# Kernel tuning notes

Measured on AMD Instinct MI355X. Metric: run time of the kernel, lower is better.

The kernel has to match this reference:

```python
import jax, jax.numpy as jnp
import numpy as np

N = 100000       # nodes
E = 1000000      # edges
NFEAT = 128
NHID = 256
NCLASS = 40
THRESHOLD = 0.1
EPS = 1e-8


def setup_inputs() -> dict:
    key = jax.random.key(0)
    k = jax.random.split(key, 5)
    x = jax.random.normal(k[0], (N, NFEAT), dtype=jnp.float32)
    row = jax.random.randint(k[1], (E,), 0, N)
    col = jax.random.randint(k[2], (E,), 0, N)
    W1 = jax.random.normal(k[3], (NFEAT, NHID), dtype=jnp.float32) / np.sqrt(NFEAT).astype(np.float32)
    b1 = jnp.zeros((NHID,), jnp.float32)
    W2 = jax.random.normal(k[4], (NHID, NCLASS), dtype=jnp.float32) / np.sqrt(NHID).astype(np.float32)
    b2 = jnp.zeros((NCLASS,), jnp.float32)
    return {"x": x, "row": row, "col": col, "W1": W1, "b1": b1, "W2": W2, "b2": b2}


def _att_coef(feat, row, col, prev_mask=None):
    # per-edge cosine similarity (F.cosine_similarity semantics, eps=1e-8)
    nrm = jnp.maximum(jnp.linalg.norm(feat, axis=1), EPS)  # [N]
    dots = jnp.sum(feat[row] * feat[col], axis=1)          # [E] gather-heavy
    sims = dots / (nrm[row] * nrm[col])
    mask = (sims >= THRESHOLD) & (row != col)
    if prev_mask is not None:
        # edges dropped by a previous att_coef no longer exist in the adj
        mask = mask & prev_mask
    # torch.no_grad in original -> weights are constants
    w = jax.lax.stop_gradient(jnp.where(mask, sims, 0.0))
    return w, mask


def _gcn_conv(x, row, col, w, W, b):
    # PyG GCNConv(add_self_loops=True, normalize=True) with edge weights w.
    # Zero-weight edges are exactly equivalent to removed edges.
    h = x @ W                                             # [N, out]
    deg = jnp.zeros((N,), h.dtype).at[row].add(w) + 1.0   # + self-loop weight 1
    dinv = jax.lax.rsqrt(deg)
    norm = dinv[row] * w * dinv[col]                      # [E]
    out = jnp.zeros((N, h.shape[1]), h.dtype).at[row].add(norm[:, None] * h[col])
    out = out + (dinv * dinv)[:, None] * h                # self-loop contribution
    return out + b


def reference(x, row, col, W1, b1, W2, b2):
    w1, m1 = _att_coef(x, row, col)
    h = _gcn_conv(x, row, col, w1, W1, b1)
    h = jax.nn.relu(h)
    # dropout in eval mode -> identity
    w2, _ = _att_coef(h, row, col, prev_mask=m1)
    out = _gcn_conv(h, row, col, w2, W2, b2)
    return out
```

## Files before the change

kernel.cpp:

```cpp
#include <hip/hip_runtime.h>
#include <hip/hip_bf16.h>
#include <hip/hip_fp16.h>

#define NFEAT 128
#define NHID  256
#define NCLASS 40
#define THRESH 0.1f
#define FEPS   1e-8f
#define GUARD2 4e-3f
#define NSTRIPE 384

struct h2x2 { __half2 a, b; };

typedef _Float16 v2h __attribute__((ext_vector_type(2)));
typedef _Float16 v8h __attribute__((ext_vector_type(8)));
typedef float f32x4 __attribute__((ext_vector_type(4)));

__device__ __forceinline__ float dot2acc(unsigned int a, unsigned int b, float s) {
#if __has_builtin(__builtin_amdgcn_fdot2)
    return __builtin_amdgcn_fdot2(__builtin_bit_cast(v2h, a),
                                  __builtin_bit_cast(v2h, b), s, false);
#else
    float2 fa = __half22float2(__builtin_bit_cast(__half2, a));
    float2 fb = __half22float2(__builtin_bit_cast(__half2, b));
    return s + fa.x * fb.x + fa.y * fb.y;
#endif
}

__device__ __forceinline__ int dot4acc(int a, int b, int acc) {
#if __has_builtin(__builtin_amdgcn_sdot4)
    return __builtin_amdgcn_sdot4(a, b, acc, false);
#else
#pragma unroll
    for (int k = 0; k < 4; ++k) {
        int av = (a << (24 - 8 * k)) >> 24;
        int bv = (b << (24 - 8 * k)) >> 24;
        acc += av * bv;
    }
    return acc;
#endif
}

__device__ __forceinline__ float waveSum(float v) {
#pragma unroll
    for (int off = 32; off > 0; off >>= 1) v += __shfl_xor(v, off, 64);
    return v;
}

__device__ __forceinline__ float qSum16(float v) {
#pragma unroll
    for (int off = 8; off > 0; off >>= 1) v += __shfl_xor(v, off, 64);
    return v;
}

__device__ __forceinline__ float waveMax(float v) {
#pragma unroll
    for (int off = 32; off > 0; off >>= 1) v = fmaxf(v, __shfl_xor(v, off, 64));
    return v;
}

__global__ void k_prep(const float* __restrict__ x,
                       signed char* __restrict__ xq, signed char* __restrict__ xql,
                       float4* __restrict__ meta,
                       float* __restrict__ nrm, float* __restrict__ deg,
                       float* __restrict__ deg2,
                       int* __restrict__ counts, float* __restrict__ nrmsq, int N) {
    int r = (blockIdx.x * blockDim.x + threadIdx.x) >> 6;
    int lane = threadIdx.x & 63;
    if (r >= N) return;
    float2 a = ((const float2*)(x + (size_t)r * NFEAT))[lane];
    float s = waveSum(a.x * a.x + a.y * a.y);
    float nr = fmaxf(sqrtf(s), FEPS);
    float inv = 1.0f / nr;
    float xn0 = a.x * inv, xn1 = a.y * inv;
    float m = waveMax(fmaxf(fabsf(xn0), fabsf(xn1)));
    float t = (m > 0.f) ? 127.f / m : 0.f;
    float sc = m * (1.0f / 127.f);
    int q0 = __float2int_rn(xn0 * t), q1 = __float2int_rn(xn1 * t);
    q0 = max(-127, min(127, q0));
    q1 = max(-127, min(127, q1));
    char2 pk; pk.x = (signed char)q0; pk.y = (signed char)q1;
    ((char2*)(xq + (size_t)r * NFEAT))[lane] = pk;
    float rq = (m > 0.f) ? 256.0f / sc : 0.f;
    int l0 = __float2int_rn((xn0 - sc * (float)q0) * rq);
    int l1 = __float2int_rn((xn1 - sc * (float)q1) * rq);
    l0 = max(-128, min(127, l0));
    l1 = max(-128, min(127, l1));
    char2 pl; pl.x = (signed char)l0; pl.y = (signed char)l1;
    ((char2*)(xql + (size_t)r * NFEAT))[lane] = pl;
    float asum = waveSum((float)(abs(q0) + abs(q1)));
    float axn  = waveSum(fabsf(xn0) + fabsf(xn1));
    if (lane == 0) {
        meta[r] = make_float4(sc, 0.5f * asum + 33.0f, axn, 0.0f);
        nrm[r] = nr;
        deg[r] = 0.0f;
        deg2[r] = 0.0f;
        counts[r] = 0;
        nrmsq[r] = 0.0f;
    }
}

__global__ void k_w1frag(const float* __restrict__ W1f, v8h* __restrict__ w1x) {
    int id = blockIdx.x * 256 + threadIdx.x;
    int frag = id >> 6, lane = id & 63;
    int kb = frag >> 4, ct = frag & 15;
    int kbase = kb * 32 + (lane >> 4) * 8;
    int n = ct * 16 + (lane & 15);
    v8h v;
#pragma unroll
    for (int j = 0; j < 8; ++j)
        v[j] = (_Float16)W1f[(size_t)(kbase + j) * NHID + n];
    w1x[id] = v;
}

__global__ void k_w2frag(const float* __restrict__ W2f, v8h* __restrict__ w2x) {
    int id = blockIdx.x * 256 + threadIdx.x;
    if (id >= 3072) return;
    int part = (id >= 1536) ? 1 : 0;
    int fid = id - part * 1536;
    int frag = fid >> 6, lane = fid & 63;
    int kb = frag / 3, ct = frag % 3;
    int kbase = kb * 32 + (lane >> 4) * 8;
    int n = ct * 16 + (lane & 15);
    v8h v;
#pragma unroll
    for (int j = 0; j < 8; ++j) {
        float wv = (n < NCLASS) ? W2f[(size_t)(kbase + j) * NCLASS + n] : 0.0f;
        _Float16 hi = (_Float16)wv;
        v[j] = part ? (_Float16)(wv - (float)hi) : hi;
    }
    w2x[id] = v;
}

__global__ void k_att1(const float* __restrict__ xf,
                       const signed char* __restrict__ xq,
                       const signed char* __restrict__ xql,
                       const float4* __restrict__ meta,
                       const int* __restrict__ row, const int* __restrict__ col,
                       const float* __restrict__ nrm,
                       float* __restrict__ w1, float* __restrict__ deg,
                       int* __restrict__ counts, int E) {
    int wid = (blockIdx.x * blockDim.x + threadIdx.x) >> 6;
    int lane = threadIdx.x & 63;
    int l8 = lane & 7;
    int e = wid * 8 + (lane >> 3);
    if (e >= E) return;
    int r = row[e], c = col[e];
    int4 qa = ((const int4*)(xq + (size_t)r * NFEAT))[l8];
    int4 qb = ((const int4*)(xq + (size_t)c * NFEAT))[l8];
    int d = 0;
    d = dot4acc(qa.x, qb.x, d);
    d = dot4acc(qa.y, qb.y, d);
    d = dot4acc(qa.z, qb.z, d);
    d = dot4acc(qa.w, qb.w, d);
    d += __shfl_xor(d, 1, 64);
    d += __shfl_xor(d, 2, 64);
    d += __shfl_xor(d, 4, 64);
    float4 mr = meta[r], mc = meta[c];
    float ub = mr.x * mc.x * ((float)d + mr.y + mc.y);
    float sims = 0.0f;
    bool alive = (ub >= THRESH - 1e-5f);
    if (alive) {
        int4 la = ((const int4*)(xql + (size_t)r * NFEAT))[l8];
        int4 lb = ((const int4*)(xql + (size_t)c * NFEAT))[l8];
        int dll = 0, dx = 0;
        dll = dot4acc(la.x, lb.x, dll); dll = dot4acc(la.y, lb.y, dll);
        dll = dot4acc(la.z, lb.z, dll); dll = dot4acc(la.w, lb.w, dll);
        dx = dot4acc(qa.x, lb.x, dx); dx = dot4acc(qa.y, lb.y, dx);
        dx = dot4acc(qa.z, lb.z, dx); dx = dot4acc(qa.w, lb.w, dx);
        dx = dot4acc(la.x, qb.x, dx); dx = dot4acc(la.y, qb.y, dx);
        dx = dot4acc(la.z, qb.z, dx); dx = dot4acc(la.w, qb.w, dx);
        int conf = dx * 256 + dll;
        conf += __shfl_xor(conf, 1, 64);
        conf += __shfl_xor(conf, 2, 64);
        conf += __shfl_xor(conf, 4, 64);
        float ss = mr.x * mc.x;
        sims = ss * ((float)d + (float)conf * (1.0f / 65536.f));
        float errB = (mr.x * mc.z + mc.x * mr.z) * (1.0f / 256.f) + ss * 0.01f + 2e-5f;
        if (__builtin_expect(fabsf(sims - THRESH) < errB, 0)) {
            const float4* fr = (const float4*)(xf + (size_t)r * NFEAT);
            const float4* fc = (const float4*)(xf + (size_t)c * NFEAT);
            float s2 = 0.f;
#pragma unroll
            for (int j = 0; j < 4; ++j) {
                float4 av = fr[l8 + 8 * j], bv = fc[l8 + 8 * j];
                s2 += av.x * bv.x + av.y * bv.y + av.z * bv.z + av.w * bv.w;
            }
            s2 += __shfl_xor(s2, 1, 64);
            s2 += __shfl_xor(s2, 2, 64);
            s2 += __shfl_xor(s2, 4, 64);
            sims = s2 / (nrm[r] * nrm[c]);
        }
    }
    if (l8 == 0) {
        float w = (alive && sims >= THRESH && r != c) ? sims : 0.0f;
        w1[e] = w;
        if (w != 0.0f) {
            unsafeAtomicAdd(&deg[r], w);
            atomicAdd(&counts[r], 1);
        }
    }
}

__global__ __launch_bounds__(256) void k_scan1(const int* __restrict__ counts,
                                               int* __restrict__ rowptr,
                                               int* __restrict__ bsum, int N) {
    __shared__ int tmp[256];
    int t = threadIdx.x, i = blockIdx.x * 256 + t;
    int v = (i < N) ? counts[i] : 0;
    tmp[t] = v;
    __syncthreads();
    for (int off = 1; off < 256; off <<= 1) {
        int add = (t >= off) ? tmp[t - off] : 0;
        __syncthreads();
        tmp[t] += add;
        __syncthreads();
    }
    if (i < N) rowptr[i] = tmp[t] - v;
    if (t == 255) bsum[blockIdx.x] = tmp[t];
}

__global__ __launch_bounds__(512) void k_scan2(int* __restrict__ bsum, int nb) {
    __shared__ int tmp[512];
    int t = threadIdx.x;
    int v = (t < nb) ? bsum[t] : 0;
    tmp[t] = v;
    __syncthreads();
    for (int off = 1; off < 512; off <<= 1) {
        int add = (t >= off) ? tmp[t - off] : 0;
        __syncthreads();
        tmp[t] += add;
        __syncthreads();
    }
    if (t < nb) bsum[t] = tmp[t] - v;
}

__global__ void k_scan3(int* __restrict__ rowptr, const int* __restrict__ bsum, int N) {
    int i = blockIdx.x * 256 + threadIdx.x;
    if (i < N) rowptr[i] += bsum[blockIdx.x];
}

__global__ void k_fill(const int* __restrict__ row, const int* __restrict__ col,
                       const float* __restrict__ wbuf, const float* __restrict__ deg,
                       int* __restrict__ rowptr, int2* __restrict__ edata, int E) {
    int e = blockIdx.x * blockDim.x + threadIdx.x;
    if (e >= E) return;
    float w = wbuf[e];
    if (w == 0.0f) return;
    int r = row[e], c = col[e];
    float dr = 1.0f / sqrtf(1.0f + deg[r]);
    float dc = 1.0f / sqrtf(1.0f + deg[c]);
    float nm = dr * w * dc;
    int pos = atomicAdd(&rowptr[r], 1);
    edata[pos] = make_int2(c, __float_as_int(nm));
}

__global__ void k_fillsrc(const int* __restrict__ rowptr, const int* __restrict__ counts,
                          int* __restrict__ esrc, int N) {
    int r = blockIdx.x * 256 + threadIdx.x;
    if (r >= N) return;
    int cnt = counts[r];
    int start = rowptr[r] - cnt;
    for (int k = 0; k < cnt; ++k) esrc[start + k] = r;
}

__global__ void k_gather1(const float* __restrict__ xf, const int* __restrict__ rowptr,
                          const int* __restrict__ counts, const float* __restrict__ deg,
                          const int2* __restrict__ edata, float* __restrict__ xagg, int N) {
    int r = (blockIdx.x * blockDim.x + threadIdx.x) >> 6;
    int lane = threadIdx.x & 63;
    if (r >= N) return;
    int cnt = counts[r];
    int start = rowptr[r] - cnt;
    float d = 1.0f / sqrtf(1.0f + deg[r]);
    float2 xa = ((const float2*)(xf + (size_t)r * NFEAT))[lane];
    float2 acc = make_float2(d * d * xa.x, d * d * xa.y);
    for (int k = 0; k < cnt; ++k) {
        int2 ed = edata[start + k];
        float nm = __int_as_float(ed.y);
        float2 xv = ((const float2*)(xf + (size_t)ed.x * NFEAT))[lane];
        acc.x += nm * xv.x;
        acc.y += nm * xv.y;
    }
    ((float2*)(xagg + (size_t)r * NFEAT))[lane] = acc;
}

__global__ __launch_bounds__(256) void k_gemm1h(const float* __restrict__ xagg,
                                                const v8h* __restrict__ w1x,
                                                const float* __restrict__ b1f,
                                                __half* __restrict__ hh16,
                                                float* __restrict__ nrmsq, int N) {
    __shared__ __half2 xsh[64][68];
    __shared__ v8h bsh[4][8][64];
    int tid = threadIdx.x;
    int ch = blockIdx.x & 1;
    int stripe = blockIdx.x >> 1;

#pragma unroll
    for (int it = 0; it < 8; ++it) {
        int id = it * 256 + tid;
        int lane = id & 63, fr = id >> 6;
        int kb = fr >> 3, ctl = fr & 7;
        bsh[kb][ctl][lane] = w1x[(size_t)(kb * 16 + ch * 8 + ctl) * 64 + lane];
    }

    int w = tid >> 6, lane = tid & 63;
    int c = lane & 15, q = lane >> 4;
    int nb = w * 16;

    int T = (N + 63) >> 6;
    for (int t = stripe; t < T; t += NSTRIPE) {
        int i0 = t * 64;
        __syncthreads();

#pragma unroll
        for (int it = 0; it < 16; ++it) {
            int idx = it * 256 + tid;
            int n = idx >> 6, kq = idx & 63;
            int i = i0 + n;
            float2 v = make_float2(0.f, 0.f);
            if (i < N) v = ((const float2*)(xagg + (size_t)i * NFEAT))[kq];
            xsh[n][kq] = __floats2half2_rn(v.x, v.y);
        }
        __syncthreads();

        f32x4 acc[8];
#pragma unroll
        for (int ct = 0; ct < 8; ++ct) acc[ct] = (f32x4){0.f, 0.f, 0.f, 0.f};

#pragma unroll
        for (int kb = 0; kb < 4; ++kb) {
            v8h a = *((const v8h*)&xsh[nb + c][kb * 16 + q * 4]);
#pragma unroll
            for (int ctl = 0; ctl < 8; ++ctl) {
                acc[ctl] = __builtin_amdgcn_mfma_f32_16x16x32_f16(
                    a, bsh[kb][ctl][lane], acc[ctl], 0, 0, 0);
            }
        }

        float s2[4] = {0.f, 0.f, 0.f, 0.f};
        bool full = (i0 + 64 <= N);
#pragma unroll
        for (int ctl = 0; ctl < 8; ++ctl) {
            int n = (ch * 8 + ctl) * 16 + c;
            float bias = b1f[n];
            f32x4 d = acc[ctl];
#pragma unroll
            for (int reg = 0; reg < 4; ++reg) {
                int node = i0 + nb + q * 4 + reg;
                float v = fmaxf(d[reg] + bias, 0.f);
                s2[reg] += v * v;
                if (full || node < N) hh16[(size_t)node * NHID + n] = __float2half(v);
            }
        }
#pragma unroll
        for (int off = 1; off < 16; off <<= 1) {
#pragma unroll
            for (int reg = 0; reg < 4; ++reg) s2[reg] += __shfl_xor(s2[reg], off, 64);
        }
        if (c == 0) {
            int base = i0 + nb + q * 4;
#pragma unroll
            for (int reg = 0; reg < 4; ++reg)
                if (base + reg < N) unsafeAtomicAdd(&nrmsq[base + reg], s2[reg]);
        }
    }
}

__global__ __launch_bounds__(256) void k_att2e(
        const float* __restrict__ xagg, const float* __restrict__ W1f,
        const float* __restrict__ b1f, const __half2* __restrict__ hh,
        const int* __restrict__ esrc, const int2* __restrict__ edata,
        const float* __restrict__ nrmsq, const int* __restrict__ etot,
        float* __restrict__ w2csr, float* __restrict__ deg2) {
    int lane = threadIdx.x & 63;
    int l16 = lane & 15, g = lane >> 4;
    int wid0 = (blockIdx.x * blockDim.x + threadIdx.x) >> 6;
    int step = (gridDim.x * blockDim.x) >> 4;
    int total = *etot;
    for (int base = wid0 * 4; base < total; base += step) {
        int pos = base + g;
        bool active = (pos < total);
        int r = 0, c = 0;
        float sims = 0.f, inv = 0.f;
        if (active) {
            r = esrc[pos];
            c = edata[pos].x;
            const uint4* hr4 = (const uint4*)(hh + (size_t)r * (NHID / 2));
            const uint4* hc4 = (const uint4*)(hh + (size_t)c * (NHID / 2));
            uint4 a0 = hr4[l16], a1 = hr4[l16 + 16];
            uint4 b0 = hc4[l16], b1 = hc4[l16 + 16];
            float s = 0.f;
            s = dot2acc(a0.x, b0.x, s); s = dot2acc(a0.y, b0.y, s);
            s = dot2acc(a0.z, b0.z, s); s = dot2acc(a0.w, b0.w, s);
            s = dot2acc(a1.x, b1.x, s); s = dot2acc(a1.y, b1.y, s);
            s = dot2acc(a1.z, b1.z, s); s = dot2acc(a1.w, b1.w, s);
            s = qSum16(s);
            float nr = fmaxf(sqrtf(nrmsq[r]), FEPS);
            float nc = fmaxf(sqrtf(nrmsq[c]), FEPS);
            inv = 1.0f / (nr * nc);
            sims = s * inv;
        }
        unsigned long long gm =
            __ballot(active && l16 == 0 && fabsf(sims - THRESH) < GUARD2);
        while (gm) {
            int src = __ffsll(gm) - 1;
            gm &= gm - 1;
            int rr = __shfl(r, src, 64);
            int cc = __shfl(c, src, 64);
            float invv = __shfl(inv, src, 64);
            int j0 = lane * 4;
            float aR[4], aC[4];
#pragma unroll
            for (int q = 0; q < 4; ++q) { aR[q] = b1f[j0 + q]; aC[q] = b1f[j0 + q]; }
            const float* xr = xagg + (size_t)rr * NFEAT;
            const float* xc = xagg + (size_t)cc * NFEAT;
            for (int kk = 0; kk < NFEAT; ++kk) {
                float vr = xr[kk], vc = xc[kk];
                float4 wv = *((const float4*)(W1f + (size_t)kk * NHID + j0));
                aR[0] += vr * wv.x; aC[0] += vc * wv.x;
                aR[1] += vr * wv.y; aC[1] += vc * wv.y;
                aR[2] += vr * wv.z; aC[2] += vc * wv.z;
                aR[3] += vr * wv.w; aC[3] += vc * wv.w;
            }
            float dp = 0.f;
#pragma unroll
            for (int q = 0; q < 4; ++q)
                dp += fmaxf(aR[q], 0.f) * fmaxf(aC[q], 0.f);
            float se = waveSum(dp) * invv;
            if (lane == src) sims = se;
        }
        if (active && l16 == 0) {
            float w2 = (sims >= THRESH) ? sims : 0.f;
            w2csr[pos] = w2;
            if (w2 != 0.f) unsafeAtomicAdd(&deg2[r], w2);
        }
    }
}

__global__ void k_dinv2(const float* __restrict__ deg2, float* __restrict__ dinv2, int N) {
    int i = blockIdx.x * 256 + threadIdx.x;
    if (i < N) dinv2[i] = 1.0f / sqrtf(1.0f + deg2[i]);
}

__global__ __launch_bounds__(256) void k_gemm2m(const __half2* __restrict__ hh,
                                                const v8h* __restrict__ w2x,
                                                float* __restrict__ g, int N) {
    __shared__ __half2 hs[64][NHID / 2 + 4];
    int tid = threadIdx.x;
    int i0 = blockIdx.x * 64;

#pragma unroll
    for (int it = 0; it < 8; ++it) {
        int idx = it * 256 + tid;
        int n = idx >> 5, kq = idx & 31;
        int i = i0 + n;
        uint4 v = make_uint4(0u, 0u, 0u, 0u);
        if (i < N) v = ((const uint4*)(hh + (size_t)i * (NHID / 2)))[kq];
        *((uint4*)&hs[n][kq * 4]) = v;
    }
    __syncthreads();

    int w = tid >> 6, lane = tid & 63;
    int c = lane & 15, q = lane >> 4;
    int nb = w * 16;

    f32x4 acc[3];
#pragma unroll
    for (int t = 0; t < 3; ++t) acc[t] = (f32x4){0.f, 0.f, 0.f, 0.f};

#pragma unroll
    for (int kb = 0; kb < 8; ++kb) {
        v8h a = *((const v8h*)&hs[nb + c][kb * 16 + q * 4]);
        const v8h* bh = w2x + (size_t)(kb * 3) * 64 + lane;
        const v8h* bl = bh + 1536;
#pragma unroll
        for (int ct = 0; ct < 3; ++ct) {
            acc[ct] = __builtin_amdgcn_mfma_f32_16x16x32_f16(a, bh[ct * 64], acc[ct], 0, 0, 0);
            acc[ct] = __builtin_amdgcn_mfma_f32_16x16x32_f16(a, bl[ct * 64], acc[ct], 0, 0, 0);
        }
    }

    bool full = (i0 + 64 <= N);
#pragma unroll
    for (int ct = 0; ct < 3; ++ct) {
        int cls = ct * 16 + c;
        if (cls < NCLASS) {
            f32x4 d = acc[ct];
#pragma unroll
            for (int reg = 0; reg < 4; ++reg) {
                int node = i0 + nb + q * 4 + reg;
                if (full || node < N) g[(size_t)node * NCLASS + cls] = d[reg];
            }
        }
    }
}

__global__ void k_gather2(const float* __restrict__ g, const int* __restrict__ rowptr,
                          const int* __restrict__ counts, const float* __restrict__ dinv2,
                          const float* __restrict__ b2f, const int2* __restrict__ edata,
                          const float* __restrict__ w2csr, float* __restrict__ out, int N) {
    int r = (blockIdx.x * blockDim.x + threadIdx.x) >> 6;
    int lane = threadIdx.x & 63;
    if (r >= N || lane >= NCLASS) return;
    int cnt = counts[r];
    int start = rowptr[r] - cnt;
    float dr = dinv2[r];
    float acc = dr * dr * g[(size_t)r * NCLASS + lane] + b2f[lane];
    for (int k = 0; k < cnt; ++k) {
        int c = edata[start + k].x;
        float w2 = w2csr[start + k];
        acc += dr * w2 * dinv2[c] * g[(size_t)c * NCLASS + lane];
    }
    out[(size_t)r * NCLASS + lane] = acc;
}

extern "C" void kernel_launch(void* const* d_in, const int* in_sizes, int n_in,
                              void* d_out, int out_size, void* d_ws, size_t ws_size,
                              hipStream_t stream) {
    const float* x  = (const float*)d_in[0];
    const int* row  = (const int*)d_in[1];
    const int* col  = (const int*)d_in[2];
    const float* W1 = (const float*)d_in[3];
    const float* b1 = (const float*)d_in[4];
    const float* W2 = (const float*)d_in[5];
    const float* b2 = (const float*)d_in[6];
    float* out = (float*)d_out;
    const int N = in_sizes[0] / NFEAT;
    const int E = in_sizes[1];

    char* ws = (char*)d_ws;
    size_t off = 0;
    auto alloc = [&](size_t bytes) {
        char* p = ws + off;
        off += (bytes + 255) & ~(size_t)255;
        return p;
    };
    float*   xagg   = (float*)alloc((size_t)N * NFEAT * 4);
    __half2* hh     = (__half2*)alloc((size_t)N * NHID * 2);
    float*   w1buf  = (float*)alloc((size_t)E * 4);
    float*   w2csr  = (float*)alloc((size_t)E * 4);
    int2*    edata  = (int2*)alloc((size_t)E * 8);
    float*   nrm    = (float*)alloc((size_t)N * 4);
    float*   deg    = (float*)alloc((size_t)N * 4);
    float*   dinv2  = (float*)alloc((size_t)N * 4);
    int*     counts = (int*)alloc((size_t)N * 4);
    int*     rowptr = (int*)alloc((size_t)N * 4);
    int*     bsum   = (int*)alloc(512 * 4);
    v8h*     w1x    = (v8h*)alloc(4096 * 16);
    v8h*     w2x    = (v8h*)alloc(3072 * 16);
    float*   nrmsq  = (float*)alloc((size_t)N * 4);
    float*   deg2   = (float*)alloc((size_t)N * 4);
    float*   g      = xagg;
    signed char* xq  = (signed char*)xagg;
    float4*  meta    = (float4*)(xq + (size_t)N * 128);
    signed char* xql = xq + (size_t)N * 144;
    int*     esrc   = (int*)w1buf;

    const int e8Blocks = (E + 31) / 32;
    const int eBlocks1 = (E + 255) / 256;
    const int nBlocks4 = (N + 3) / 4;
    const int scanB    = (N + 255) / 256;

    k_prep<<<nBlocks4, 256, 0, stream>>>(x, xq, xql, meta, nrm, deg, deg2, counts,
                                         nrmsq, N);
    k_w1frag<<<16, 256, 0, stream>>>(W1, w1x);
    k_w2frag<<<12, 256, 0, stream>>>(W2, w2x);
    k_att1<<<e8Blocks, 256, 0, stream>>>(x, xq, xql, meta, row, col, nrm, w1buf, deg,
                                         counts, E);
    k_scan1<<<scanB, 256, 0, stream>>>(counts, rowptr, bsum, N);
    k_scan2<<<1, 512, 0, stream>>>(bsum, scanB);
    k_scan3<<<scanB, 256, 0, stream>>>(rowptr, bsum, N);
    k_fill<<<eBlocks1, 256, 0, stream>>>(row, col, w1buf, deg, rowptr, edata, E);
    k_fillsrc<<<scanB, 256, 0, stream>>>(rowptr, counts, esrc, N);
    k_gather1<<<nBlocks4, 256, 0, stream>>>(x, rowptr, counts, deg, edata, xagg, N);
    k_gemm1h<<<2 * NSTRIPE, 256, 0, stream>>>(xagg, w1x, b1, (__half*)hh, nrmsq, N);

    k_att2e<<<4096, 256, 0, stream>>>(xagg, W1, b1, hh, esrc, edata, nrmsq,
                                      rowptr + (N - 1), w2csr, deg2);
    k_dinv2<<<scanB, 256, 0, stream>>>(deg2, dinv2, N);
    k_gemm2m<<<(N + 63) / 64, 256, 0, stream>>>(hh, w2x, g, N);
    k_gather2<<<nBlocks4, 256, 0, stream>>>(g, rowptr, counts, dinv2, b2, edata, w2csr,
                                            out, N);
}
```

Baseline: 338.1 us.

## Narrow lanes per edge/row in attention and gather kernels, fuse esrc fill

Several kernels now give each edge or row fewer lanes, and each lane does more work. k_att1 uses 4 lanes per edge instead of 8, k_att2e uses 8 instead of 16, and k_gather1/k_gather2 use 8 lanes per row instead of a full wave. This is meant to raise memory-level parallelism, cut shuffle-reduction steps, and avoid idle lanes in gather2, where only 40 of 64 lanes were active. k_fillsrc is removed and esrc is written inside k_fill, which drops a serial per-row loop and a launch but adds a separate E-sized buffer and more scattered writes. Wider per-lane loads raise register use and may reduce coalescing.

```diff
diff --git a/kernel.cpp b/kernel.cpp
--- a/kernel.cpp
+++ b/kernel.cpp
@@ -9,8 +9,6 @@
 #define FEPS   1e-8f
 #define GUARD2 4e-3f
 #define NSTRIPE 384
-
-struct h2x2 { __half2 a, b; };
 
 typedef _Float16 v2h __attribute__((ext_vector_type(2)));
 typedef _Float16 v8h __attribute__((ext_vector_type(8)));
@@ -44,12 +42,6 @@
 __device__ __forceinline__ float waveSum(float v) {
 #pragma unroll
     for (int off = 32; off > 0; off >>= 1) v += __shfl_xor(v, off, 64);
-    return v;
-}
-
-__device__ __forceinline__ float qSum16(float v) {
-#pragma unroll
-    for (int off = 8; off > 0; off >>= 1) v += __shfl_xor(v, off, 64);
     return v;
 }
 
@@ -142,38 +134,46 @@
                        int* __restrict__ counts, int E) {
     int wid = (blockIdx.x * blockDim.x + threadIdx.x) >> 6;
     int lane = threadIdx.x & 63;
-    int l8 = lane & 7;
-    int e = wid * 8 + (lane >> 3);
+    int l4 = lane & 3;
+    int e = wid * 16 + (lane >> 2);
     if (e >= E) return;
     int r = row[e], c = col[e];
-    int4 qa = ((const int4*)(xq + (size_t)r * NFEAT))[l8];
-    int4 qb = ((const int4*)(xq + (size_t)c * NFEAT))[l8];
+    const int4* qra = (const int4*)(xq + (size_t)r * NFEAT);
+    const int4* qca = (const int4*)(xq + (size_t)c * NFEAT);
+    int4 qa0 = qra[l4 * 2], qa1 = qra[l4 * 2 + 1];
+    int4 qb0 = qca[l4 * 2], qb1 = qca[l4 * 2 + 1];
     int d = 0;
-    d = dot4acc(qa.x, qb.x, d);
-    d = dot4acc(qa.y, qb.y, d);
-    d = dot4acc(qa.z, qb.z, d);
-    d = dot4acc(qa.w, qb.w, d);
+    d = dot4acc(qa0.x, qb0.x, d); d = dot4acc(qa0.y, qb0.y, d);
+    d = dot4acc(qa0.z, qb0.z, d); d = dot4acc(qa0.w, qb0.w, d);
+    d = dot4acc(qa1.x, qb1.x, d); d = dot4acc(qa1.y, qb1.y, d);
+    d = dot4acc(qa1.z, qb1.z, d); d = dot4acc(qa1.w, qb1.w, d);
     d += __shfl_xor(d, 1, 64);
     d += __shfl_xor(d, 2, 64);
-    d += __shfl_xor(d, 4, 64);
     float4 mr = meta[r], mc = meta[c];
     float ub = mr.x * mc.x * ((float)d + mr.y + mc.y);
     float sims = 0.0f;
     bool alive = (ub >= THRESH - 1e-5f);
     if (alive) {
-        int4 la = ((const int4*)(xql + (size_t)r * NFEAT))[l8];
-        int4 lb = ((const int4*)(xql + (size_t)c * NFEAT))[l8];
+        const int4* lra = (const int4*)(xql + (size_t)r * NFEAT);
+        const int4* lca = (const int4*)(xql + (size_t)c * NFEAT);
+        int4 la0 = lra[l4 * 2], la1 = lra[l4 * 2 + 1];
+        int4 lb0 = lca[l4 * 2], lb1 = lca[l4 * 2 + 1];
         int dll = 0, dx = 0;
-        dll = dot4acc(la.x, lb.x, dll); dll = dot4acc(la.y, lb.y, dll);
-        dll = dot4acc(la.z, lb.z, dll); dll = dot4acc(la.w, lb.w, dll);
-        dx = dot4acc(qa.x, lb.x, dx); dx = dot4acc(qa.y, lb.y, dx);
-        dx = dot4acc(qa.z, lb.z, dx); dx = dot4acc(qa.w, lb.w, dx);
-        dx = dot4acc(la.x, qb.x, dx); dx = dot4acc(la.y, qb.y, dx);
-        dx = dot4acc(la.z, qb.z, dx); dx = dot4acc(la.w, qb.w, dx);
+        dll = dot4acc(la0.x, lb0.x, dll); dll = dot4acc(la0.y, lb0.y, dll);
+        dll = dot4acc(la0.z, lb0.z, dll); dll = dot4acc(la0.w, lb0.w, dll);
+        dll = dot4acc(la1.x, lb1.x, dll); dll = dot4acc(la1.y, lb1.y, dll);
+        dll = dot4acc(la1.z, lb1.z, dll); dll = dot4acc(la1.w, lb1.w, dll);
+        dx = dot4acc(qa0.x, lb0.x, dx); dx = dot4acc(qa0.y, lb0.y, dx);
+        dx = dot4acc(qa0.z, lb0.z, dx); dx = dot4acc(qa0.w, lb0.w, dx);
+        dx = dot4acc(qa1.x, lb1.x, dx); dx = dot4acc(qa1.y, lb1.y, dx);
+        dx = dot4acc(qa1.z, lb1.z, dx); dx = dot4acc(qa1.w, lb1.w, dx);
+        dx = dot4acc(la0.x, qb0.x, dx); dx = dot4acc(la0.y, qb0.y, dx);
+        dx = dot4acc(la0.z, qb0.z, dx); dx = dot4acc(la0.w, qb0.w, dx);
+        dx = dot4acc(la1.x, qb1.x, dx); dx = dot4acc(la1.y, qb1.y, dx);
+        dx = dot4acc(la1.z, qb1.z, dx); dx = dot4acc(la1.w, qb1.w, dx);
         int conf = dx * 256 + dll;
         conf += __shfl_xor(conf, 1, 64);
         conf += __shfl_xor(conf, 2, 64);
-        conf += __shfl_xor(conf, 4, 64);
         float ss = mr.x * mc.x;
         sims = ss * ((float)d + (float)conf * (1.0f / 65536.f));
         float errB = (mr.x * mc.z + mc.x * mr.z) * (1.0f / 256.f) + ss * 0.01f + 2e-5f;
@@ -182,17 +182,16 @@
             const float4* fc = (const float4*)(xf + (size_t)c * NFEAT);
             float s2 = 0.f;
 #pragma unroll
-            for (int j = 0; j < 4; ++j) {
-                float4 av = fr[l8 + 8 * j], bv = fc[l8 + 8 * j];
+            for (int j = 0; j < 8; ++j) {
+                float4 av = fr[l4 + 4 * j], bv = fc[l4 + 4 * j];
                 s2 += av.x * bv.x + av.y * bv.y + av.z * bv.z + av.w * bv.w;
             }
             s2 += __shfl_xor(s2, 1, 64);
             s2 += __shfl_xor(s2, 2, 64);
-            s2 += __shfl_xor(s2, 4, 64);
             sims = s2 / (nrm[r] * nrm[c]);
         }
     }
-    if (l8 == 0) {
+    if (l4 == 0) {
         float w = (alive && sims >= THRESH && r != c) ? sims : 0.0f;
         w1[e] = w;
         if (w != 0.0f) {
@@ -242,7 +241,8 @@
 
 __global__ void k_fill(const int* __restrict__ row, const int* __restrict__ col,
                        const float* __restrict__ wbuf, const float* __restrict__ deg,
-                       int* __restrict__ rowptr, int2* __restrict__ edata, int E) {
+                       int* __restrict__ rowptr, int2* __restrict__ edata,
+                       int* __restrict__ esrc, int E) {
     int e = blockIdx.x * blockDim.x + threadIdx.x;
     if (e >= E) return;
     float w = wbuf[e];
@@ -253,36 +253,41 @@
     float nm = dr * w * dc;
     int pos = atomicAdd(&rowptr[r], 1);
     edata[pos] = make_int2(c, __float_as_int(nm));
-}
-
-__global__ void k_fillsrc(const int* __restrict__ rowptr, const int* __restrict__ counts,
-                          int* __restrict__ esrc, int N) {
-    int r = blockIdx.x * 256 + threadIdx.x;
-    if (r >= N) return;
-    int cnt = counts[r];
-    int start = rowptr[r] - cnt;
-    for (int k = 0; k < cnt; ++k) esrc[start + k] = r;
+    esrc[pos] = r;
 }
 
 __global__ void k_gather1(const float* __restrict__ xf, const int* __restrict__ rowptr,
                           const int* __restrict__ counts, const float* __restrict__ deg,
                           const int2* __restrict__ edata, float* __restrict__ xagg, int N) {
-    int r = (blockIdx.x * blockDim.x + threadIdx.x) >> 6;
-    int lane = threadIdx.x & 63;
+    int tid = blockIdx.x * blockDim.x + threadIdx.x;
+    int r = tid >> 3;
+    int l = tid & 7;
     if (r >= N) return;
     int cnt = counts[r];
     int start = rowptr[r] - cnt;
     float d = 1.0f / sqrtf(1.0f + deg[r]);
-    float2 xa = ((const float2*)(xf + (size_t)r * NFEAT))[lane];
-    float2 acc = make_float2(d * d * xa.x, d * d * xa.y);
+    float dd = d * d;
+    const float4* xr = (const float4*)(xf + (size_t)r * NFEAT) + l * 4;
+    float4 c0, c1, c2, c3;
+    {
+        float4 a0 = xr[0], a1 = xr[1], a2 = xr[2], a3 = xr[3];
+        c0 = make_float4(dd * a0.x, dd * a0.y, dd * a0.z, dd * a0.w);
+        c1 = make_float4(dd * a1.x, dd * a1.y, dd * a1.z, dd * a1.w);
+        c2 = make_float4(dd * a2.x, dd * a2.y, dd * a2.z, dd * a2.w);
+        c3 = make_float4(dd * a3.x, dd * a3.y, dd * a3.z, dd * a3.w);
+    }
     for (int k = 0; k < cnt; ++k) {
         int2 ed = edata[start + k];
         float nm = __int_as_float(ed.y);
-        float2 xv = ((const float2*)(xf + (size_t)ed.x * NFEAT))[lane];
-        acc.x += nm * xv.x;
-        acc.y += nm * xv.y;
-    }
-    ((float2*)(xagg + (size_t)r * NFEAT))[lane] = acc;
+        const float4* xc = (const float4*)(xf + (size_t)ed.x * NFEAT) + l * 4;
+        float4 b0 = xc[0], b1 = xc[1], b2 = xc[2], b3 = xc[3];
+        c0.x += nm * b0.x; c0.y += nm * b0.y; c0.z += nm * b0.z; c0.w += nm * b0.w;
+        c1.x += nm * b1.x; c1.y += nm * b1.y; c1.z += nm * b1.z; c1.w += nm * b1.w;
+        c2.x += nm * b2.x; c2.y += nm * b2.y; c2.z += nm * b2.z; c2.w += nm * b2.w;
+        c3.x += nm * b3.x; c3.y += nm * b3.y; c3.z += nm * b3.z; c3.w += nm * b3.w;
+    }
+    float4* xo = (float4*)(xagg + (size_t)r * NFEAT) + l * 4;
+    xo[0] = c0; xo[1] = c1; xo[2] = c2; xo[3] = c3;
 }
 
 __global__ __launch_bounds__(256) void k_gemm1h(const float* __restrict__ xagg,
@@ -374,11 +379,11 @@
         const float* __restrict__ nrmsq, const int* __restrict__ etot,
         float* __restrict__ w2csr, float* __restrict__ deg2) {
     int lane = threadIdx.x & 63;
-    int l16 = lane & 15, g = lane >> 4;
+    int l8 = lane & 7, g = lane >> 3;
     int wid0 = (blockIdx.x * blockDim.x + threadIdx.x) >> 6;
-    int step = (gridDim.x * blockDim.x) >> 4;
+    int step = (gridDim.x * blockDim.x) >> 3;
     int total = *etot;
-    for (int base = wid0 * 4; base < total; base += step) {
+    for (int base = wid0 * 8; base < total; base += step) {
         int pos = base + g;
         bool active = (pos < total);
         int r = 0, c = 0;
@@ -388,21 +393,24 @@
             c = edata[pos].x;
             const uint4* hr4 = (const uint4*)(hh + (size_t)r * (NHID / 2));
             const uint4* hc4 = (const uint4*)(hh + (size_t)c * (NHID / 2));
-            uint4 a0 = hr4[l16], a1 = hr4[l16 + 16];
-            uint4 b0 = hc4[l16], b1 = hc4[l16 + 16];
             float s = 0.f;
-            s = dot2acc(a0.x, b0.x, s); s = dot2acc(a0.y, b0.y, s);
-            s = dot2acc(a0.z, b0.z, s); s = dot2acc(a0.w, b0.w, s);
-            s = dot2acc(a1.x, b1.x, s); s = dot2acc(a1.y, b1.y, s);
-            s = dot2acc(a1.z, b1.z, s); s = dot2acc(a1.w, b1.w, s);
-            s = qSum16(s);
+#pragma unroll
+            for (int j = 0; j < 4; ++j) {
+                uint4 a = hr4[l8 + 8 * j];
+                uint4 b = hc4[l8 + 8 * j];
+                s = dot2acc(a.x, b.x, s); s = dot2acc(a.y, b.y, s);
+                s = dot2acc(a.z, b.z, s); s = dot2acc(a.w, b.w, s);
+            }
+            s += __shfl_xor(s, 1, 64);
+            s += __shfl_xor(s, 2, 64);
+            s += __shfl_xor(s, 4, 64);
             float nr = fmaxf(sqrtf(nrmsq[r]), FEPS);
             float nc = fmaxf(sqrtf(nrmsq[c]), FEPS);
             inv = 1.0f / (nr * nc);
             sims = s * inv;
         }
         unsigned long long gm =
-            __ballot(active && l16 == 0 && fabsf(sims - THRESH) < GUARD2);
+            __ballot(active && l8 == 0 && fabsf(sims - THRESH) < GUARD2);
         while (gm) {
             int src = __ffsll(gm) - 1;
             gm &= gm - 1;
@@ -430,7 +438,7 @@
             float se = waveSum(dp) * invv;
             if (lane == src) sims = se;
         }
-        if (active && l16 == 0) {
+        if (active && l8 == 0) {
             float w2 = (sims >= THRESH) ? sims : 0.f;
             w2csr[pos] = w2;
             if (w2 != 0.f) unsafeAtomicAdd(&deg2[r], w2);
@@ -500,19 +508,29 @@
                           const int* __restrict__ counts, const float* __restrict__ dinv2,
                           const float* __restrict__ b2f, const int2* __restrict__ edata,
                           const float* __restrict__ w2csr, float* __restrict__ out, int N) {
-    int r = (blockIdx.x * blockDim.x + threadIdx.x) >> 6;
-    int lane = threadIdx.x & 63;
-    if (r >= N || lane >= NCLASS) return;
+    int tid = blockIdx.x * blockDim.x + threadIdx.x;
+    int r = tid >> 3;
+    int l = tid & 7;
+    if (r >= N) return;
     int cnt = counts[r];
     int start = rowptr[r] - cnt;
     float dr = dinv2[r];
-    float acc = dr * dr * g[(size_t)r * NCLASS + lane] + b2f[lane];
+    float drr = dr * dr;
+    const float* gr = g + (size_t)r * NCLASS;
+    float acc[5];
+#pragma unroll
+    for (int q = 0; q < 5; ++q) acc[q] = drr * gr[l + 8 * q] + b2f[l + 8 * q];
     for (int k = 0; k < cnt; ++k) {
-        int c = edata[start + k].x;
+        int2 ed = edata[start + k];
         float w2 = w2csr[start + k];
-        acc += dr * w2 * dinv2[c] * g[(size_t)c * NCLASS + lane];
-    }
-    out[(size_t)r * NCLASS + lane] = acc;
+        float f = dr * w2 * dinv2[ed.x];
+        const float* gc = g + (size_t)ed.x * NCLASS;
+#pragma unroll
+        for (int q = 0; q < 5; ++q) acc[q] += f * gc[l + 8 * q];
+    }
+    float* po = out + (size_t)r * NCLASS;
+#pragma unroll
+    for (int q = 0; q < 5; ++q) po[l + 8 * q] = acc[q];
 }
 
 extern "C" void kernel_launch(void* const* d_in, const int* in_sizes, int n_in,
@@ -541,6 +559,7 @@
     float*   w1buf  = (float*)alloc((size_t)E * 4);
     float*   w2csr  = (float*)alloc((size_t)E * 4);
     int2*    edata  = (int2*)alloc((size_t)E * 8);
+    int*     esrc   = (int*)alloc((size_t)E * 4);
     float*   nrm    = (float*)alloc((size_t)N * 4);
     float*   deg    = (float*)alloc((size_t)N * 4);
     float*   dinv2  = (float*)alloc((size_t)N * 4);
@@ -555,31 +574,30 @@
     signed char* xq  = (signed char*)xagg;
     float4*  meta    = (float4*)(xq + (size_t)N * 128);
     signed char* xql = xq + (size_t)N * 144;
-    int*     esrc   = (int*)w1buf;
-
-    const int e8Blocks = (E + 31) / 32;
+
+    const int e16Blocks = (E + 63) / 64;
     const int eBlocks1 = (E + 255) / 256;
     const int nBlocks4 = (N + 3) / 4;
+    const int nBlocks8 = (N + 31) / 32;
     const int scanB    = (N + 255) / 256;
 
     k_prep<<<nBlocks4, 256, 0, stream>>>(x, xq, xql, meta, nrm, deg, deg2, counts,
                                          nrmsq, N);
     k_w1frag<<<16, 256, 0, stream>>>(W1, w1x);
     k_w2frag<<<12, 256, 0, stream>>>(W2, w2x);
-    k_att1<<<e8Blocks, 256, 0, stream>>>(x, xq, xql, meta, row, col, nrm, w1buf, deg,
-                                         counts, E);
+    k_att1<<<e16Blocks, 256, 0, stream>>>(x, xq, xql, meta, row, col, nrm, w1buf, deg,
+                                          counts, E);
     k_scan1<<<scanB, 256, 0, stream>>>(counts, rowptr, bsum, N);
     k_scan2<<<1, 512, 0, stream>>>(bsum, scanB);
     k_scan3<<<scanB, 256, 0, stream>>>(rowptr, bsum, N);
-    k_fill<<<eBlocks1, 256, 0, stream>>>(row, col, w1buf, deg, rowptr, edata, E);
-    k_fillsrc<<<scanB, 256, 0, stream>>>(rowptr, counts, esrc, N);
-    k_gather1<<<nBlocks4, 256, 0, stream>>>(x, rowptr, counts, deg, edata, xagg, N);
+    k_fill<<<eBlocks1, 256, 0, stream>>>(row, col, w1buf, deg, rowptr, edata, esrc, E);
+    k_gather1<<<nBlocks8, 256, 0, stream>>>(x, rowptr, counts, deg, edata, xagg, N);
     k_gemm1h<<<2 * NSTRIPE, 256, 0, stream>>>(xagg, w1x, b1, (__half*)hh, nrmsq, N);
 
     k_att2e<<<4096, 256, 0, stream>>>(xagg, W1, b1, hh, esrc, edata, nrmsq,
                                       rowptr + (N - 1), w2csr, deg2);
     k_dinv2<<<scanB, 256, 0, stream>>>(deg2, dinv2, N);
     k_gemm2m<<<(N + 63) / 64, 256, 0, stream>>>(hh, w2x, g, N);
-    k_gather2<<<nBlocks4, 256, 0, stream>>>(g, rowptr, counts, dinv2, b2, edata, w2csr,
+    k_gather2<<<nBlocks8, 256, 0, stream>>>(g, rowptr, counts, dinv2, b2, edata, w2csr,
                                             out, N);
 }
```

Result: faster. 315.7 us (-6.6%).
